# Optimization experiments

Hardware: AMD Instinct MI355X
Metric: run time of the kernel (lower is better)

## Reference

```python
import jax, jax.numpy as jnp
import numpy as np
import math

DIM_IN = 512
DIM_OUT = 512
KERNEL = 3
STYLE_DIM = 2 * 128
LIN_SCALE = 1.0 / math.sqrt(STYLE_DIM)      # EqualLinear scale (lr_mul=1)
CONV_SCALE = 1.0 / math.sqrt(DIM_IN * KERNEL ** 2)  # fan_in = dim_in * k**2 (as in source)
PAD = KERNEL // 2


def setup_inputs() -> dict:
    key = jax.random.key(0)
    ks = jax.random.split(key, 5)
    B, T = 16, 2048
    x = jax.random.normal(ks[0], (B, DIM_IN, T), dtype=jnp.float32)
    c_src = jax.random.normal(ks[1], (B, 128), dtype=jnp.float32)
    c_trg = jax.random.normal(ks[2], (B, 128), dtype=jnp.float32)
    style_w = jax.random.normal(ks[3], (DIM_IN, STYLE_DIM), dtype=jnp.float32)
    style_b = jnp.ones((DIM_IN,), dtype=jnp.float32)  # bias_init=1
    weight = jax.random.normal(ks[4], (1, DIM_OUT, DIM_IN, KERNEL), dtype=jnp.float32)
    return {"x": x, "c_src": c_src, "c_trg": c_trg,
            "style_w": style_w, "style_b": style_b, "weight": weight}


def reference(x, c_src, c_trg, style_w, style_b, weight):
    B = x.shape[0]
    # EqualLinear: style code s [B, dim_in]
    c = jnp.concatenate([c_src, c_trg], axis=-1)              # [B, 256]
    s = c @ (style_w * LIN_SCALE).T + style_b                 # [B, dim_in]
    # Modulate: w [B, dim_out, dim_in, k]
    w = CONV_SCALE * weight * s[:, None, :, None]
    # Demodulate over (dim_in, k)
    demod = jax.lax.rsqrt(jnp.sum(w * w, axis=(2, 3)) + 1e-8)  # [B, dim_out]
    w = w * demod[:, :, None, None]
    # Per-sample conv1d, padding 'same' (pad = k//2), vmapped over batch
    def conv1(xi, wi):
        # xi: [dim_in, T], wi: [dim_out, dim_in, k]
        out = jax.lax.conv_general_dilated(
            xi[None], wi, window_strides=(1,), padding=[(PAD, PAD)],
            dimension_numbers=("NCH", "OIH", "NCH"))
        return out[0]                                          # [dim_out, T]
    return jax.vmap(conv1)(x, w)                               # [B, dim_out, T]
```

## Files before the change

### kernel.cpp

```cpp
#include <hip/hip_runtime.h>
#include <cstdint>
#include <cstddef>


#define LIN_SCALE  0.0625f
#define CONV_SCALE 0.014731391f

#define B_   16
#define CIN  512
#define COUT 512
#define T_   2048
#define TP   2050

typedef __bf16 bf16x8 __attribute__((ext_vector_type(8)));
typedef float  f32x4  __attribute__((ext_vector_type(4)));
typedef unsigned short u16x8 __attribute__((ext_vector_type(8)));
typedef unsigned short u16x2 __attribute__((ext_vector_type(2)));

#define AS1 __attribute__((address_space(1)))
#define AS3 __attribute__((address_space(3)))

__device__ inline unsigned short f2bf(float f) {
  __bf16 h = (__bf16)f;
  return __builtin_bit_cast(unsigned short, h);
}

__global__ __launch_bounds__(256) void style_kernel(const float* __restrict__ c_src,
                                                    const float* __restrict__ c_trg,
                                                    const float* __restrict__ sw,
                                                    const float* __restrict__ sb,
                                                    float* __restrict__ s) {
  __shared__ float c[256];
  const int b = blockIdx.y;
  const int tid = threadIdx.x;
  c[tid] = (tid < 128) ? c_src[b * 128 + tid] : c_trg[b * 128 + tid - 128];
  __syncthreads();
  const int w = tid >> 6, lane = tid & 63;
  #pragma unroll
  for (int rr = 0; rr < 16; ++rr) {
    const int i = blockIdx.x * 64 + w * 16 + rr;
    const float* row = sw + (size_t)i * 256;
    float acc = row[lane] * c[lane] + row[lane + 64] * c[lane + 64]
              + row[lane + 128] * c[lane + 128] + row[lane + 192] * c[lane + 192];
    #pragma unroll
    for (int off = 32; off; off >>= 1) acc += __shfl_down(acc, off, 64);
    if (lane == 0) s[b * 512 + i] = acc * LIN_SCALE + sb[i];
  }
}

__global__ __launch_bounds__(256) void demod_kernel(const float* __restrict__ weight,
                                                    const float* __restrict__ s,
                                                    float* __restrict__ demod,
                                                    unsigned short* __restrict__ Wb) {
  const int o = blockIdx.x;
  const int tid = threadIdx.x;
  __shared__ float wsh[1536];
  __shared__ float svs[16 * 512];
  __shared__ float partial[16][4];

  #pragma unroll
  for (int j = tid; j < 384; j += 256)
    ((float4*)wsh)[j] = ((const float4*)(weight + (size_t)o * 1536))[j];
  #pragma unroll
  for (int j = tid; j < 2048; j += 256)
    ((float4*)svs)[j] = ((const float4*)s)[j];
  __syncthreads();

  float wr[6];
  #pragma unroll
  for (int q = 0; q < 6; ++q) wr[q] = wsh[tid * 6 + q] * CONV_SCALE;

  #pragma unroll
  for (int k = 0; k < 3; ++k) {
    u16x2 v;
    v.x = f2bf(wr[k]);
    v.y = f2bf(wr[3 + k]);
    *(u16x2*)&Wb[((size_t)(k * 512 + o)) * 512 + 2 * tid] = v;
  }

  const int lane = tid & 63, w = tid >> 6;
  float ssb[16];
  #pragma unroll
  for (int b = 0; b < 16; ++b) {
    const float s0 = svs[b * 512 + 2 * tid];
    const float s1 = svs[b * 512 + 2 * tid + 1];
    float ss = 0.f;
    #pragma unroll
    for (int q = 0; q < 3; ++q) { float v = wr[q] * s0; ss += v * v; }
    #pragma unroll
    for (int q = 3; q < 6; ++q) { float v = wr[q] * s1; ss += v * v; }
    ssb[b] = ss;
  }
  #pragma unroll
  for (int b = 0; b < 16; ++b) {
    float ss = ssb[b];
    #pragma unroll
    for (int off = 32; off; off >>= 1) ss += __shfl_down(ss, off, 64);
    if (lane == 0) partial[b][w] = ss;
  }
  __syncthreads();
  if (tid < 16)
    demod[(size_t)tid * 512 + o] =
        rsqrtf(partial[tid][0] + partial[tid][1] + partial[tid][2] + partial[tid][3] + 1e-8f);
}

__global__ __launch_bounds__(256) void transpose_kernel(const float* __restrict__ x,
                                                        const float* __restrict__ s,
                                                        unsigned short* __restrict__ xT) {
  __shared__ float tile[64][65];
  __shared__ float ss[64];
  const int b = blockIdx.z, i0 = blockIdx.y * 64, t0 = blockIdx.x * 64;
  const int tid = threadIdx.x;

  if (tid < 64) ss[tid] = s[(size_t)b * 512 + i0 + tid];

  const int lr = tid >> 4;
  const int lc = (tid & 15) * 4;
  const float* xb = x + ((size_t)b * CIN + i0) * T_ + t0;
  #pragma unroll
  for (int p = 0; p < 4; ++p) {
    const int r = p * 16 + lr;
    const float4 v = *(const float4*)(xb + (size_t)r * T_ + lc);
    tile[r][lc + 0] = v.x; tile[r][lc + 1] = v.y;
    tile[r][lc + 2] = v.z; tile[r][lc + 3] = v.w;
  }
  if (blockIdx.x == 0 && tid < 8)
    *(u16x8*)&xT[(size_t)b * TP * CIN + i0 + tid * 8] = (u16x8){0,0,0,0,0,0,0,0};
  if (blockIdx.x == gridDim.x - 1 && tid < 8)
    *(u16x8*)&xT[((size_t)b * TP + TP - 1) * CIN + i0 + tid * 8] = (u16x8){0,0,0,0,0,0,0,0};
  __syncthreads();

  const int st = tid >> 3;
  const int si = (tid & 7) * 8;
  float sv[8];
  #pragma unroll
  for (int q = 0; q < 8; ++q) sv[q] = ss[si + q];
  unsigned short* xTb = xT + ((size_t)b * TP + 1 + t0) * CIN + i0;
  #pragma unroll
  for (int p = 0; p < 2; ++p) {
    const int t = p * 32 + st;
    u16x8 v;
    #pragma unroll
    for (int q = 0; q < 8; ++q) v[q] = f2bf(tile[si + q][t] * sv[q]);
    *(u16x8*)&xTb[(size_t)t * CIN + si] = v;
  }
}

#define BM 128
#define BN 256
#define BK 32

__global__ __launch_bounds__(256, 2) void gemm_kernel(const unsigned short* __restrict__ Wb,
                                                      const unsigned short* __restrict__ xT,
                                                      const float* __restrict__ demod,
                                                      float* __restrict__ out) {
  __shared__ unsigned short lA[3 * 128 * 32];
  __shared__ unsigned short lB[258 * 32];

  const int id  = blockIdx.x;
  const int xcd = id & 7;
  const int j   = id >> 3;
  const int b   = xcd + 8 * (j >> 5);
  const int r   = j & 31;
  const int o0  = (r >> 3) * BM;
  const int t0  = (r & 7) * BN;

  const int tid  = threadIdx.x;
  const int lane = tid & 63;
  const int wm   = ((tid >> 6) & 1) * 64;
  const int wn   = (tid >> 7) * 128;
  const int rl   = lane & 15;
  const int kc   = lane >> 4;

  const unsigned short* gW = Wb + (size_t)o0 * 512;
  const unsigned short* gX = xT + ((size_t)b * TP + t0) * CIN;

  f32x4 acc[4][8];
  #pragma unroll
  for (int i = 0; i < 4; ++i)
    #pragma unroll
    for (int jj = 0; jj < 8; ++jj) acc[i][jj] = (f32x4){0.f, 0.f, 0.f, 0.f};

  for (int kk = 0; kk < 16; ++kk) {
    const int i0 = kk * 32;
    __syncthreads();
    #pragma unroll
    for (int q = 0; q < 6; ++q) {
      const int ci  = q * 256 + tid;
      const int row = ci >> 2;
      const int tap = row >> 7;
      const int ar  = row & 127;
      const int gc  = ((ci & 3) ^ ((ar >> 1) & 3)) * 8;
      __builtin_amdgcn_global_load_lds(
          (const AS1 void*)(gW + (size_t)tap * 262144 + (size_t)ar * 512 + i0 + gc),
          (AS3 void*)(&lA[ci * 8]), 16, 0, 0);
    }
    #pragma unroll
    for (int q = 0; q < 4; ++q) {
      const int ci  = q * 256 + tid;
      const int row = ci >> 2;
      const int gc  = ((ci & 3) ^ ((row >> 1) & 3)) * 8;
      __builtin_amdgcn_global_load_lds(
          (const AS1 void*)(gX + (size_t)row * CIN + i0 + gc),
          (AS3 void*)(&lB[ci * 8]), 16, 0, 0);
    }
    if (tid < 8) {
      const int ci  = 1024 + tid;
      const int row = ci >> 2;
      const int gc  = ((ci & 3) ^ ((row >> 1) & 3)) * 8;
      __builtin_amdgcn_global_load_lds(
          (const AS1 void*)(gX + (size_t)row * CIN + i0 + gc),
          (AS3 void*)(&lB[ci * 8]), 16, 0, 0);
    }
    __syncthreads();

    #pragma unroll
    for (int tap = 0; tap < 3; ++tap) {
      bf16x8 af[4], bfr[8];
      #pragma unroll
      for (int mi = 0; mi < 4; ++mi) {
        const int ra = wm + mi * 16 + rl;
        af[mi] = *(const bf16x8*)&lA[((tap * 128 + ra) * 4 + (kc ^ ((ra >> 1) & 3))) * 8];
      }
      #pragma unroll
      for (int ni = 0; ni < 8; ++ni) {
        const int rb = wn + ni * 16 + rl + tap;
        bfr[ni] = *(const bf16x8*)&lB[(rb * 4 + (kc ^ ((rb >> 1) & 3))) * 8];
      }
      #pragma unroll
      for (int mi = 0; mi < 4; ++mi)
        #pragma unroll
        for (int ni = 0; ni < 8; ++ni)
          acc[mi][ni] = __builtin_amdgcn_mfma_f32_16x16x32_bf16(af[mi], bfr[ni], acc[mi][ni], 0, 0, 0);
    }
  }

  float* ob = out + ((size_t)b * COUT + o0 + wm) * T_ + t0 + wn;
  const float* dm = demod + (size_t)b * 512 + o0 + wm;
  const int rrow = (lane >> 4) * 4;
  const int ccol = lane & 15;
  #pragma unroll
  for (int mi = 0; mi < 4; ++mi) {
    float dr[4];
    #pragma unroll
    for (int rr = 0; rr < 4; ++rr) dr[rr] = dm[mi * 16 + rrow + rr];
    #pragma unroll
    for (int ni = 0; ni < 8; ++ni)
      #pragma unroll
      for (int rr = 0; rr < 4; ++rr)
        ob[(size_t)(mi * 16 + rrow + rr) * T_ + ni * 16 + ccol] = acc[mi][ni][rr] * dr[rr];
  }
}

extern "C" void kernel_launch(void* const* d_in, const int* in_sizes, int n_in,
                              void* d_out, int out_size, void* d_ws, size_t ws_size,
                              hipStream_t stream) {
  const float* x       = (const float*)d_in[0];
  const float* c_src   = (const float*)d_in[1];
  const float* c_trg   = (const float*)d_in[2];
  const float* style_w = (const float*)d_in[3];
  const float* style_b = (const float*)d_in[4];
  const float* weight  = (const float*)d_in[5];
  float* out = (float*)d_out;

  char* ws = (char*)d_ws;
  float* s_buf          = (float*)ws;
  float* demod_buf      = (float*)(ws + 32768);
  unsigned short* Wb    = (unsigned short*)(ws + 65536);
  unsigned short* xTbuf = (unsigned short*)(ws + 65536 + 1572864);

  style_kernel<<<dim3(8, 16), 256, 0, stream>>>(c_src, c_trg, style_w, style_b, s_buf);
  demod_kernel<<<dim3(COUT), 256, 0, stream>>>(weight, s_buf, demod_buf, Wb);
  transpose_kernel<<<dim3(T_ / 64, CIN / 64, B_), 256, 0, stream>>>(x, s_buf, xTbuf);
  gemm_kernel<<<dim3(512), 256, 0, stream>>>(Wb, xTbuf, demod_buf, out);
}
```

Baseline: 181.3 us.

## Double-buffer GEMM LDS stages with 512-thread blocks and per-tap prefetch interleaving

The GEMM kernel now uses 512-thread blocks covering a 128x512 output tile and double-buffered LDS. The next k-slice's A and B tiles are fetched asynchronously, interleaved with the three tap MFMA phases, and ordered with explicit vmcnt waits and barriers. MFMA sections are raised to higher priority, and demod values are preloaded before the main loop. The aim is to hide global-to-LDS latency behind compute and reuse each weight tile over a wider time tile. In exchange, LDS use doubles, the grid halves to 256 blocks, and correctness now relies on hand-tuned waitcnt values.

```diff
diff --git a/kernel.cpp b/kernel.cpp
--- a/kernel.cpp
+++ b/kernel.cpp
@@ -147,109 +147,153 @@
 }
 
 #define BM 128
-#define BN 256
-#define BK 32
-
-__global__ __launch_bounds__(256, 2) void gemm_kernel(const unsigned short* __restrict__ Wb,
+#define BN 512
+
+#define VMCNT(n) asm volatile("s_waitcnt vmcnt(" #n ")" ::: "memory")
+#define LGKM0    asm volatile("s_waitcnt lgkmcnt(0)" ::: "memory")
+#define BAR()    __builtin_amdgcn_s_barrier()
+#define SB()     __builtin_amdgcn_sched_barrier(0)
+
+#define STAGE_B(buf, i0g)                                                     \
+  { _Pragma("unroll")                                                         \
+    for (int q = 0; q < 4; ++q) {                                             \
+      const int ci  = q * 512 + tid;                                          \
+      const int row = ci >> 2;                                                \
+      const int gc  = ((ci & 3) ^ ((row >> 1) & 3)) * 8;                      \
+      __builtin_amdgcn_global_load_lds(                                       \
+          (const AS1 void*)(gX + (size_t)row * CIN + (i0g) + gc),             \
+          (AS3 void*)(&lB[buf][ci * 8]), 16, 0, 0);                           \
+    }                                                                         \
+    if (lane == 0) {                                                          \
+      const int ci  = 2048 + wid;                                             \
+      const int row = 512 + (wid >> 2);                                       \
+      const int gc  = ((ci & 3) ^ ((row >> 1) & 3)) * 8;                      \
+      __builtin_amdgcn_global_load_lds(                                       \
+          (const AS1 void*)(gX + (size_t)row * CIN + (i0g) + gc),             \
+          (AS3 void*)(&lB[buf][ci * 8]), 16, 0, 0);                           \
+    } }
+
+#define STAGE_A(buf, i0g, q)                                                  \
+  { const int ci  = (q) * 512 + tid;                                          \
+    const int ar  = tid >> 2;                                                 \
+    const int gc  = ((ci & 3) ^ ((ar >> 1) & 3)) * 8;                         \
+    __builtin_amdgcn_global_load_lds(                                         \
+        (const AS1 void*)(gW + (size_t)(q) * 262144 + (size_t)ar * 512 + (i0g) + gc), \
+        (AS3 void*)(&lA[buf][ci * 8]), 16, 0, 0);                             \
+  }
+
+#define FRAGS(tap)                                                            \
+  bf16x8 af[4]; bf16x8 bfr[8];                                                \
+  { const unsigned short* La = &lA[cur][0];                                   \
+    const unsigned short* Lb = &lB[cur][0];                                   \
+    _Pragma("unroll")                                                         \
+    for (int mi = 0; mi < 4; ++mi) {                                          \
+      const int ra = wm + mi * 16 + rl;                                       \
+      af[mi] = *(const bf16x8*)&La[(((tap) * 128 + ra) * 4 + (kc ^ ((ra >> 1) & 3))) * 8]; \
+    }                                                                         \
+    _Pragma("unroll")                                                         \
+    for (int ni = 0; ni < 8; ++ni) {                                          \
+      const int rb = wn + ni * 16 + rl + (tap);                               \
+      bfr[ni] = *(const bf16x8*)&Lb[(rb * 4 + (kc ^ ((rb >> 1) & 3))) * 8];   \
+    } }
+
+#define MFMAS()                                                               \
+  __builtin_amdgcn_s_setprio(1);                                              \
+  _Pragma("unroll")                                                           \
+  for (int mi = 0; mi < 4; ++mi)                                              \
+    _Pragma("unroll")                                                         \
+    for (int ni = 0; ni < 8; ++ni)                                            \
+      acc[mi][ni] = __builtin_amdgcn_mfma_f32_16x16x32_bf16(af[mi], bfr[ni], acc[mi][ni], 0, 0, 0); \
+  __builtin_amdgcn_s_setprio(0);
+
+__global__ __launch_bounds__(512, 2) void gemm_kernel(const unsigned short* __restrict__ Wb,
                                                       const unsigned short* __restrict__ xT,
                                                       const float* __restrict__ demod,
                                                       float* __restrict__ out) {
-  __shared__ unsigned short lA[3 * 128 * 32];
-  __shared__ unsigned short lB[258 * 32];
+  __shared__ unsigned short lA[2][1536 * 8];
+  __shared__ unsigned short lB[2][2056 * 8];
 
   const int id  = blockIdx.x;
   const int xcd = id & 7;
   const int j   = id >> 3;
-  const int b   = xcd + 8 * (j >> 5);
-  const int r   = j & 31;
-  const int o0  = (r >> 3) * BM;
-  const int t0  = (r & 7) * BN;
+  const int b   = xcd + 8 * (j >> 4);
+  const int r   = j & 15;
+  const int o0  = (r >> 2) * BM;
+  const int t0  = (r & 3) * BN;
 
   const int tid  = threadIdx.x;
   const int lane = tid & 63;
-  const int wm   = ((tid >> 6) & 1) * 64;
-  const int wn   = (tid >> 7) * 128;
+  const int wid  = tid >> 6;
+  const int wm   = (wid & 1) * 64;
+  const int wn   = (wid >> 1) * 128;
   const int rl   = lane & 15;
   const int kc   = lane >> 4;
 
   const unsigned short* gW = Wb + (size_t)o0 * 512;
   const unsigned short* gX = xT + ((size_t)b * TP + t0) * CIN;
 
+  float dmv[16];
+  {
+    const float* dmp = demod + (size_t)b * 512 + o0 + wm + (lane >> 4) * 4;
+    #pragma unroll
+    for (int mi = 0; mi < 4; ++mi)
+      #pragma unroll
+      for (int rr = 0; rr < 4; ++rr) dmv[mi * 4 + rr] = dmp[mi * 16 + rr];
+  }
+
   f32x4 acc[4][8];
   #pragma unroll
   for (int i = 0; i < 4; ++i)
     #pragma unroll
     for (int jj = 0; jj < 8; ++jj) acc[i][jj] = (f32x4){0.f, 0.f, 0.f, 0.f};
 
-  for (int kk = 0; kk < 16; ++kk) {
-    const int i0 = kk * 32;
-    __syncthreads();
-    #pragma unroll
-    for (int q = 0; q < 6; ++q) {
-      const int ci  = q * 256 + tid;
-      const int row = ci >> 2;
-      const int tap = row >> 7;
-      const int ar  = row & 127;
-      const int gc  = ((ci & 3) ^ ((ar >> 1) & 3)) * 8;
-      __builtin_amdgcn_global_load_lds(
-          (const AS1 void*)(gW + (size_t)tap * 262144 + (size_t)ar * 512 + i0 + gc),
-          (AS3 void*)(&lA[ci * 8]), 16, 0, 0);
+  STAGE_B(0, 0);
+  STAGE_A(0, 0, 0);
+  STAGE_A(0, 0, 1);
+  STAGE_A(0, 0, 2);
+  VMCNT(2); BAR(); SB();
+
+  for (int kk = 0; kk < 15; ++kk) {
+    const int cur = kk & 1;
+    const int nxt = cur ^ 1;
+    const int i0n = (kk + 1) * 32;
+    {
+      FRAGS(0);
+      STAGE_B(nxt, i0n);
+      VMCNT(6); BAR(); SB(); LGKM0; SB();
+      MFMAS(); BAR(); SB();
     }
-    #pragma unroll
-    for (int q = 0; q < 4; ++q) {
-      const int ci  = q * 256 + tid;
-      const int row = ci >> 2;
-      const int gc  = ((ci & 3) ^ ((row >> 1) & 3)) * 8;
-      __builtin_amdgcn_global_load_lds(
-          (const AS1 void*)(gX + (size_t)row * CIN + i0 + gc),
-          (AS3 void*)(&lB[ci * 8]), 16, 0, 0);
+    {
+      FRAGS(1);
+      STAGE_A(nxt, i0n, 0);
+      STAGE_A(nxt, i0n, 1);
+      VMCNT(7); BAR(); SB(); LGKM0; SB();
+      MFMAS(); BAR(); SB();
     }
-    if (tid < 8) {
-      const int ci  = 1024 + tid;
-      const int row = ci >> 2;
-      const int gc  = ((ci & 3) ^ ((row >> 1) & 3)) * 8;
-      __builtin_amdgcn_global_load_lds(
-          (const AS1 void*)(gX + (size_t)row * CIN + i0 + gc),
-          (AS3 void*)(&lB[ci * 8]), 16, 0, 0);
+    {
+      FRAGS(2);
+      STAGE_A(nxt, i0n, 2);
+      VMCNT(2); BAR(); SB(); LGKM0; SB();
+      MFMAS(); BAR(); SB();
     }
-    __syncthreads();
-
-    #pragma unroll
-    for (int tap = 0; tap < 3; ++tap) {
-      bf16x8 af[4], bfr[8];
-      #pragma unroll
-      for (int mi = 0; mi < 4; ++mi) {
-        const int ra = wm + mi * 16 + rl;
-        af[mi] = *(const bf16x8*)&lA[((tap * 128 + ra) * 4 + (kc ^ ((ra >> 1) & 3))) * 8];
-      }
-      #pragma unroll
-      for (int ni = 0; ni < 8; ++ni) {
-        const int rb = wn + ni * 16 + rl + tap;
-        bfr[ni] = *(const bf16x8*)&lB[(rb * 4 + (kc ^ ((rb >> 1) & 3))) * 8];
-      }
-      #pragma unroll
-      for (int mi = 0; mi < 4; ++mi)
-        #pragma unroll
-        for (int ni = 0; ni < 8; ++ni)
-          acc[mi][ni] = __builtin_amdgcn_mfma_f32_16x16x32_bf16(af[mi], bfr[ni], acc[mi][ni], 0, 0, 0);
-    }
+  }
+  {
+    const int cur = 1;
+    { FRAGS(0); VMCNT(1); BAR(); SB(); LGKM0; SB(); MFMAS(); BAR(); SB(); }
+    { FRAGS(1); VMCNT(0); BAR(); SB(); LGKM0; SB(); MFMAS(); BAR(); SB(); }
+    { FRAGS(2); LGKM0; SB(); MFMAS(); }
   }
 
   float* ob = out + ((size_t)b * COUT + o0 + wm) * T_ + t0 + wn;
-  const float* dm = demod + (size_t)b * 512 + o0 + wm;
   const int rrow = (lane >> 4) * 4;
   const int ccol = lane & 15;
   #pragma unroll
-  for (int mi = 0; mi < 4; ++mi) {
-    float dr[4];
-    #pragma unroll
-    for (int rr = 0; rr < 4; ++rr) dr[rr] = dm[mi * 16 + rrow + rr];
+  for (int mi = 0; mi < 4; ++mi)
     #pragma unroll
     for (int ni = 0; ni < 8; ++ni)
       #pragma unroll
       for (int rr = 0; rr < 4; ++rr)
-        ob[(size_t)(mi * 16 + rrow + rr) * T_ + ni * 16 + ccol] = acc[mi][ni][rr] * dr[rr];
-  }
+        ob[(size_t)(mi * 16 + rrow + rr) * T_ + ni * 16 + ccol] = acc[mi][ni][rr] * dmv[mi * 4 + rr];
 }
 
 extern "C" void kernel_launch(void* const* d_in, const int* in_sizes, int n_in,
@@ -272,5 +316,5 @@
   style_kernel<<<dim3(8, 16), 256, 0, stream>>>(c_src, c_trg, style_w, style_b, s_buf);
   demod_kernel<<<dim3(COUT), 256, 0, stream>>>(weight, s_buf, demod_buf, Wb);
   transpose_kernel<<<dim3(T_ / 64, CIN / 64, B_), 256, 0, stream>>>(x, s_buf, xTbuf);
-  gemm_kernel<<<dim3(512), 256, 0, stream>>>(Wb, xTbuf, demod_buf, out);
-}
+  gemm_kernel<<<dim3(256), 512, 0, stream>>>(Wb, xTbuf, demod_buf, out);
+}
```

Result: slower. 185.0 us (+2.1%).

## Fuse style, transpose, demod and GEMM into one persistent kernel with grid barriers

Applied to the files above, without the earlier changes.

Replaces the four kernel launches with a single 512-block kernel that runs the style linear, the scaled transpose of x, the demod/weight conversion and the conv GEMM in phases. The phases are separated by software grid barriers built on atomics, plus a tiny init kernel that resets the barrier counters. This removes launch gaps and the idle tail between dependent kernels. In exchange every block must be co-resident for the barrier to complete (512 blocks at 2 per CU), the barriers spin, and the transpose work is redistributed as 8 tiles per block.

```diff
diff --git a/kernel.cpp b/kernel.cpp
--- a/kernel.cpp
+++ b/kernel.cpp
@@ -25,230 +25,253 @@
   return __builtin_bit_cast(unsigned short, h);
 }
 
-__global__ __launch_bounds__(256) void style_kernel(const float* __restrict__ c_src,
-                                                    const float* __restrict__ c_trg,
-                                                    const float* __restrict__ sw,
-                                                    const float* __restrict__ sb,
-                                                    float* __restrict__ s) {
-  __shared__ float c[256];
-  const int b = blockIdx.y;
+__global__ void init_kernel(unsigned* sync) { sync[0] = 0u; sync[1] = 0u; }
+
+__device__ inline void grid_barrier(unsigned* cnt, unsigned* gen, unsigned nb) {
+  __syncthreads();
+  if (threadIdx.x == 0) {
+    __threadfence();
+    const unsigned g = __hip_atomic_load(gen, __ATOMIC_RELAXED, __HIP_MEMORY_SCOPE_AGENT);
+    const unsigned a = __hip_atomic_fetch_add(cnt, 1u, __ATOMIC_ACQ_REL, __HIP_MEMORY_SCOPE_AGENT);
+    if (a == nb - 1u) {
+      __hip_atomic_store(cnt, 0u, __ATOMIC_RELAXED, __HIP_MEMORY_SCOPE_AGENT);
+      __hip_atomic_store(gen, g + 1u, __ATOMIC_RELEASE, __HIP_MEMORY_SCOPE_AGENT);
+    } else {
+      int t = 0;
+      while (__hip_atomic_load(gen, __ATOMIC_ACQUIRE, __HIP_MEMORY_SCOPE_AGENT) == g) {
+        __builtin_amdgcn_s_sleep(2);
+        if (++t > (1 << 24)) break;
+      }
+    }
+    __threadfence();
+  }
+  __syncthreads();
+}
+
+__global__ __launch_bounds__(256, 2) void mega_kernel(
+    const float* __restrict__ x, const float* __restrict__ c_src,
+    const float* __restrict__ c_trg, const float* __restrict__ sw,
+    const float* __restrict__ sb, const float* __restrict__ weight,
+    float* __restrict__ s, float* __restrict__ demod,
+    unsigned short* __restrict__ Wb, unsigned short* __restrict__ xT,
+    float* __restrict__ out, unsigned* __restrict__ sync) {
+  __shared__ __align__(16) char smem[41472];
+  const int id  = blockIdx.x;
   const int tid = threadIdx.x;
-  c[tid] = (tid < 128) ? c_src[b * 128 + tid] : c_trg[b * 128 + tid - 128];
+
+  if (id < 128) {
+    float* c = (float*)smem;
+    const int b = id >> 3, bx = id & 7;
+    c[tid] = (tid < 128) ? c_src[b * 128 + tid] : c_trg[b * 128 + tid - 128];
+    __syncthreads();
+    const int w = tid >> 6, lane = tid & 63;
+    #pragma unroll
+    for (int rr = 0; rr < 16; ++rr) {
+      const int i = bx * 64 + w * 16 + rr;
+      const float* row = sw + (size_t)i * 256;
+      float acc = row[lane] * c[lane] + row[lane + 64] * c[lane + 64]
+                + row[lane + 128] * c[lane + 128] + row[lane + 192] * c[lane + 192];
+      #pragma unroll
+      for (int off = 32; off; off >>= 1) acc += __shfl_down(acc, off, 64);
+      if (lane == 0) s[b * 512 + i] = acc * LIN_SCALE + sb[i];
+    }
+  }
+  grid_barrier(sync, sync + 1, gridDim.x);
+
+  {
+    float* tile = (float*)smem;
+    float* ss   = (float*)(smem + 64 * 65 * 4);
+    const int b   = id >> 5;
+    const int i0  = ((id >> 2) & 7) * 64;
+    const int t0b = (id & 3) * 512;
+    if (tid < 64) ss[tid] = s[(size_t)b * 512 + i0 + tid];
+
+    const int lr = tid >> 4;
+    const int lc = (tid & 15) * 4;
+    const int st = tid >> 3;
+    const int si = (tid & 7) * 8;
+
+    for (int u = 0; u < 8; ++u) {
+      const int t0 = t0b + u * 64;
+      if (u) __syncthreads();
+      const float* xb = x + ((size_t)b * CIN + i0) * T_ + t0;
+      #pragma unroll
+      for (int p = 0; p < 4; ++p) {
+        const int r = p * 16 + lr;
+        const float4 v = *(const float4*)(xb + (size_t)r * T_ + lc);
+        tile[r * 65 + lc + 0] = v.x; tile[r * 65 + lc + 1] = v.y;
+        tile[r * 65 + lc + 2] = v.z; tile[r * 65 + lc + 3] = v.w;
+      }
+      if (t0 == 0 && tid < 8)
+        *(u16x8*)&xT[(size_t)b * TP * CIN + i0 + tid * 8] = (u16x8){0,0,0,0,0,0,0,0};
+      if (t0 == T_ - 64 && tid < 8)
+        *(u16x8*)&xT[((size_t)b * TP + TP - 1) * CIN + i0 + tid * 8] = (u16x8){0,0,0,0,0,0,0,0};
+      __syncthreads();
+      float sv[8];
+      #pragma unroll
+      for (int q = 0; q < 8; ++q) sv[q] = ss[si + q];
+      unsigned short* xTb = xT + ((size_t)b * TP + 1 + t0) * CIN + i0;
+      #pragma unroll
+      for (int p = 0; p < 2; ++p) {
+        const int t = p * 32 + st;
+        u16x8 v;
+        #pragma unroll
+        for (int q = 0; q < 8; ++q) v[q] = f2bf(tile[(si + q) * 65 + t] * sv[q]);
+        *(u16x8*)&xTb[(size_t)t * CIN + si] = v;
+      }
+    }
+  }
   __syncthreads();
-  const int w = tid >> 6, lane = tid & 63;
-  #pragma unroll
-  for (int rr = 0; rr < 16; ++rr) {
-    const int i = blockIdx.x * 64 + w * 16 + rr;
-    const float* row = sw + (size_t)i * 256;
-    float acc = row[lane] * c[lane] + row[lane + 64] * c[lane + 64]
-              + row[lane + 128] * c[lane + 128] + row[lane + 192] * c[lane + 192];
-    #pragma unroll
-    for (int off = 32; off; off >>= 1) acc += __shfl_down(acc, off, 64);
-    if (lane == 0) s[b * 512 + i] = acc * LIN_SCALE + sb[i];
-  }
-}
-
-__global__ __launch_bounds__(256) void demod_kernel(const float* __restrict__ weight,
-                                                    const float* __restrict__ s,
-                                                    float* __restrict__ demod,
-                                                    unsigned short* __restrict__ Wb) {
-  const int o = blockIdx.x;
-  const int tid = threadIdx.x;
-  __shared__ float wsh[1536];
-  __shared__ float svs[16 * 512];
-  __shared__ float partial[16][4];
-
-  #pragma unroll
-  for (int j = tid; j < 384; j += 256)
-    ((float4*)wsh)[j] = ((const float4*)(weight + (size_t)o * 1536))[j];
-  #pragma unroll
-  for (int j = tid; j < 2048; j += 256)
-    ((float4*)svs)[j] = ((const float4*)s)[j];
-  __syncthreads();
-
-  float wr[6];
-  #pragma unroll
-  for (int q = 0; q < 6; ++q) wr[q] = wsh[tid * 6 + q] * CONV_SCALE;
-
-  #pragma unroll
-  for (int k = 0; k < 3; ++k) {
-    u16x2 v;
-    v.x = f2bf(wr[k]);
-    v.y = f2bf(wr[3 + k]);
-    *(u16x2*)&Wb[((size_t)(k * 512 + o)) * 512 + 2 * tid] = v;
-  }
-
-  const int lane = tid & 63, w = tid >> 6;
-  float ssb[16];
-  #pragma unroll
-  for (int b = 0; b < 16; ++b) {
-    const float s0 = svs[b * 512 + 2 * tid];
-    const float s1 = svs[b * 512 + 2 * tid + 1];
-    float ss = 0.f;
-    #pragma unroll
-    for (int q = 0; q < 3; ++q) { float v = wr[q] * s0; ss += v * v; }
-    #pragma unroll
-    for (int q = 3; q < 6; ++q) { float v = wr[q] * s1; ss += v * v; }
-    ssb[b] = ss;
-  }
-  #pragma unroll
-  for (int b = 0; b < 16; ++b) {
-    float ss = ssb[b];
-    #pragma unroll
-    for (int off = 32; off; off >>= 1) ss += __shfl_down(ss, off, 64);
-    if (lane == 0) partial[b][w] = ss;
-  }
-  __syncthreads();
-  if (tid < 16)
-    demod[(size_t)tid * 512 + o] =
-        rsqrtf(partial[tid][0] + partial[tid][1] + partial[tid][2] + partial[tid][3] + 1e-8f);
-}
-
-__global__ __launch_bounds__(256) void transpose_kernel(const float* __restrict__ x,
-                                                        const float* __restrict__ s,
-                                                        unsigned short* __restrict__ xT) {
-  __shared__ float tile[64][65];
-  __shared__ float ss[64];
-  const int b = blockIdx.z, i0 = blockIdx.y * 64, t0 = blockIdx.x * 64;
-  const int tid = threadIdx.x;
-
-  if (tid < 64) ss[tid] = s[(size_t)b * 512 + i0 + tid];
-
-  const int lr = tid >> 4;
-  const int lc = (tid & 15) * 4;
-  const float* xb = x + ((size_t)b * CIN + i0) * T_ + t0;
-  #pragma unroll
-  for (int p = 0; p < 4; ++p) {
-    const int r = p * 16 + lr;
-    const float4 v = *(const float4*)(xb + (size_t)r * T_ + lc);
-    tile[r][lc + 0] = v.x; tile[r][lc + 1] = v.y;
-    tile[r][lc + 2] = v.z; tile[r][lc + 3] = v.w;
-  }
-  if (blockIdx.x == 0 && tid < 8)
-    *(u16x8*)&xT[(size_t)b * TP * CIN + i0 + tid * 8] = (u16x8){0,0,0,0,0,0,0,0};
-  if (blockIdx.x == gridDim.x - 1 && tid < 8)
-    *(u16x8*)&xT[((size_t)b * TP + TP - 1) * CIN + i0 + tid * 8] = (u16x8){0,0,0,0,0,0,0,0};
-  __syncthreads();
-
-  const int st = tid >> 3;
-  const int si = (tid & 7) * 8;
-  float sv[8];
-  #pragma unroll
-  for (int q = 0; q < 8; ++q) sv[q] = ss[si + q];
-  unsigned short* xTb = xT + ((size_t)b * TP + 1 + t0) * CIN + i0;
-  #pragma unroll
-  for (int p = 0; p < 2; ++p) {
-    const int t = p * 32 + st;
-    u16x8 v;
-    #pragma unroll
-    for (int q = 0; q < 8; ++q) v[q] = f2bf(tile[si + q][t] * sv[q]);
-    *(u16x8*)&xTb[(size_t)t * CIN + si] = v;
-  }
-}
-
-#define BM 128
-#define BN 256
-#define BK 32
-
-__global__ __launch_bounds__(256, 2) void gemm_kernel(const unsigned short* __restrict__ Wb,
-                                                      const unsigned short* __restrict__ xT,
-                                                      const float* __restrict__ demod,
-                                                      float* __restrict__ out) {
-  __shared__ unsigned short lA[3 * 128 * 32];
-  __shared__ unsigned short lB[258 * 32];
-
-  const int id  = blockIdx.x;
-  const int xcd = id & 7;
-  const int j   = id >> 3;
-  const int b   = xcd + 8 * (j >> 5);
-  const int r   = j & 31;
-  const int o0  = (r >> 3) * BM;
-  const int t0  = (r & 7) * BN;
-
-  const int tid  = threadIdx.x;
-  const int lane = tid & 63;
-  const int wm   = ((tid >> 6) & 1) * 64;
-  const int wn   = (tid >> 7) * 128;
-  const int rl   = lane & 15;
-  const int kc   = lane >> 4;
-
-  const unsigned short* gW = Wb + (size_t)o0 * 512;
-  const unsigned short* gX = xT + ((size_t)b * TP + t0) * CIN;
-
-  f32x4 acc[4][8];
-  #pragma unroll
-  for (int i = 0; i < 4; ++i)
-    #pragma unroll
-    for (int jj = 0; jj < 8; ++jj) acc[i][jj] = (f32x4){0.f, 0.f, 0.f, 0.f};
-
-  for (int kk = 0; kk < 16; ++kk) {
-    const int i0 = kk * 32;
+
+  {
+    float* wsh     = (float*)smem;
+    float* svs     = (float*)(smem + 6144);
+    float* partial = (float*)(smem + 38912);
+    const int o = id;
+
+    #pragma unroll
+    for (int j = tid; j < 384; j += 256)
+      ((float4*)wsh)[j] = ((const float4*)(weight + (size_t)o * 1536))[j];
+    #pragma unroll
+    for (int j = tid; j < 2048; j += 256)
+      ((float4*)svs)[j] = ((const float4*)s)[j];
     __syncthreads();
-    #pragma unroll
-    for (int q = 0; q < 6; ++q) {
-      const int ci  = q * 256 + tid;
-      const int row = ci >> 2;
-      const int tap = row >> 7;
-      const int ar  = row & 127;
-      const int gc  = ((ci & 3) ^ ((ar >> 1) & 3)) * 8;
-      __builtin_amdgcn_global_load_lds(
-          (const AS1 void*)(gW + (size_t)tap * 262144 + (size_t)ar * 512 + i0 + gc),
-          (AS3 void*)(&lA[ci * 8]), 16, 0, 0);
-    }
-    #pragma unroll
-    for (int q = 0; q < 4; ++q) {
-      const int ci  = q * 256 + tid;
-      const int row = ci >> 2;
-      const int gc  = ((ci & 3) ^ ((row >> 1) & 3)) * 8;
-      __builtin_amdgcn_global_load_lds(
-          (const AS1 void*)(gX + (size_t)row * CIN + i0 + gc),
-          (AS3 void*)(&lB[ci * 8]), 16, 0, 0);
-    }
-    if (tid < 8) {
-      const int ci  = 1024 + tid;
-      const int row = ci >> 2;
-      const int gc  = ((ci & 3) ^ ((row >> 1) & 3)) * 8;
-      __builtin_amdgcn_global_load_lds(
-          (const AS1 void*)(gX + (size_t)row * CIN + i0 + gc),
-          (AS3 void*)(&lB[ci * 8]), 16, 0, 0);
+
+    float wr[6];
+    #pragma unroll
+    for (int q = 0; q < 6; ++q) wr[q] = wsh[tid * 6 + q] * CONV_SCALE;
+
+    #pragma unroll
+    for (int k = 0; k < 3; ++k) {
+      u16x2 v;
+      v.x = f2bf(wr[k]);
+      v.y = f2bf(wr[3 + k]);
+      *(u16x2*)&Wb[((size_t)(k * 512 + o)) * 512 + 2 * tid] = v;
+    }
+
+    const int lane = tid & 63, w = tid >> 6;
+    float ssb[16];
+    #pragma unroll
+    for (int b = 0; b < 16; ++b) {
+      const float s0 = svs[b * 512 + 2 * tid];
+      const float s1 = svs[b * 512 + 2 * tid + 1];
+      float ssq = 0.f;
+      #pragma unroll
+      for (int q = 0; q < 3; ++q) { float v = wr[q] * s0; ssq += v * v; }
+      #pragma unroll
+      for (int q = 3; q < 6; ++q) { float v = wr[q] * s1; ssq += v * v; }
+      ssb[b] = ssq;
+    }
+    #pragma unroll
+    for (int b = 0; b < 16; ++b) {
+      float ssq = ssb[b];
+      #pragma unroll
+      for (int off = 32; off; off >>= 1) ssq += __shfl_down(ssq, off, 64);
+      if (lane == 0) partial[b * 4 + w] = ssq;
     }
     __syncthreads();
-
-    #pragma unroll
-    for (int tap = 0; tap < 3; ++tap) {
-      bf16x8 af[4], bfr[8];
-      #pragma unroll
-      for (int mi = 0; mi < 4; ++mi) {
-        const int ra = wm + mi * 16 + rl;
-        af[mi] = *(const bf16x8*)&lA[((tap * 128 + ra) * 4 + (kc ^ ((ra >> 1) & 3))) * 8];
-      }
-      #pragma unroll
-      for (int ni = 0; ni < 8; ++ni) {
-        const int rb = wn + ni * 16 + rl + tap;
-        bfr[ni] = *(const bf16x8*)&lB[(rb * 4 + (kc ^ ((rb >> 1) & 3))) * 8];
-      }
-      #pragma unroll
-      for (int mi = 0; mi < 4; ++mi)
-        #pragma unroll
-        for (int ni = 0; ni < 8; ++ni)
-          acc[mi][ni] = __builtin_amdgcn_mfma_f32_16x16x32_bf16(af[mi], bfr[ni], acc[mi][ni], 0, 0, 0);
-    }
-  }
-
-  float* ob = out + ((size_t)b * COUT + o0 + wm) * T_ + t0 + wn;
-  const float* dm = demod + (size_t)b * 512 + o0 + wm;
-  const int rrow = (lane >> 4) * 4;
-  const int ccol = lane & 15;
-  #pragma unroll
-  for (int mi = 0; mi < 4; ++mi) {
-    float dr[4];
-    #pragma unroll
-    for (int rr = 0; rr < 4; ++rr) dr[rr] = dm[mi * 16 + rrow + rr];
-    #pragma unroll
-    for (int ni = 0; ni < 8; ++ni)
-      #pragma unroll
-      for (int rr = 0; rr < 4; ++rr)
-        ob[(size_t)(mi * 16 + rrow + rr) * T_ + ni * 16 + ccol] = acc[mi][ni][rr] * dr[rr];
+    if (tid < 16)
+      demod[(size_t)tid * 512 + o] =
+          rsqrtf(partial[tid * 4] + partial[tid * 4 + 1] + partial[tid * 4 + 2]
+               + partial[tid * 4 + 3] + 1e-8f);
+  }
+  grid_barrier(sync, sync + 1, gridDim.x);
+
+  {
+    unsigned short* lA = (unsigned short*)smem;
+    unsigned short* lB = (unsigned short*)(smem + 24576);
+
+    const int xcd = id & 7;
+    const int j   = id >> 3;
+    const int b   = xcd + 8 * (j >> 5);
+    const int r   = j & 31;
+    const int o0  = (r >> 3) * 128;
+    const int t0  = (r & 7) * 256;
+
+    const int lane = tid & 63;
+    const int wm   = ((tid >> 6) & 1) * 64;
+    const int wn   = (tid >> 7) * 128;
+    const int rl   = lane & 15;
+    const int kc   = lane >> 4;
+
+    const unsigned short* gW = Wb + (size_t)o0 * 512;
+    const unsigned short* gX = xT + ((size_t)b * TP + t0) * CIN;
+
+    f32x4 acc[4][8];
+    #pragma unroll
+    for (int i = 0; i < 4; ++i)
+      #pragma unroll
+      for (int jj = 0; jj < 8; ++jj) acc[i][jj] = (f32x4){0.f, 0.f, 0.f, 0.f};
+
+    for (int kk = 0; kk < 16; ++kk) {
+      const int i0 = kk * 32;
+      __syncthreads();
+      #pragma unroll
+      for (int q = 0; q < 6; ++q) {
+        const int ci  = q * 256 + tid;
+        const int row = ci >> 2;
+        const int tap = row >> 7;
+        const int ar  = row & 127;
+        const int gc  = ((ci & 3) ^ ((ar >> 1) & 3)) * 8;
+        __builtin_amdgcn_global_load_lds(
+            (const AS1 void*)(gW + (size_t)tap * 262144 + (size_t)ar * 512 + i0 + gc),
+            (AS3 void*)(&lA[ci * 8]), 16, 0, 0);
+      }
+      #pragma unroll
+      for (int q = 0; q < 4; ++q) {
+        const int ci  = q * 256 + tid;
+        const int row = ci >> 2;
+        const int gc  = ((ci & 3) ^ ((row >> 1) & 3)) * 8;
+        __builtin_amdgcn_global_load_lds(
+            (const AS1 void*)(gX + (size_t)row * CIN + i0 + gc),
+            (AS3 void*)(&lB[ci * 8]), 16, 0, 0);
+      }
+      if (tid < 8) {
+        const int ci  = 1024 + tid;
+        const int row = ci >> 2;
+        const int gc  = ((ci & 3) ^ ((row >> 1) & 3)) * 8;
+        __builtin_amdgcn_global_load_lds(
+            (const AS1 void*)(gX + (size_t)row * CIN + i0 + gc),
+            (AS3 void*)(&lB[ci * 8]), 16, 0, 0);
+      }
+      __syncthreads();
+
+      #pragma unroll
+      for (int tap = 0; tap < 3; ++tap) {
+        bf16x8 af[4], bfr[8];
+        #pragma unroll
+        for (int mi = 0; mi < 4; ++mi) {
+          const int ra = wm + mi * 16 + rl;
+          af[mi] = *(const bf16x8*)&lA[((tap * 128 + ra) * 4 + (kc ^ ((ra >> 1) & 3))) * 8];
+        }
+        #pragma unroll
+        for (int ni = 0; ni < 8; ++ni) {
+          const int rb = wn + ni * 16 + rl + tap;
+          bfr[ni] = *(const bf16x8*)&lB[(rb * 4 + (kc ^ ((rb >> 1) & 3))) * 8];
+        }
+        #pragma unroll
+        for (int mi = 0; mi < 4; ++mi)
+          #pragma unroll
+          for (int ni = 0; ni < 8; ++ni)
+            acc[mi][ni] = __builtin_amdgcn_mfma_f32_16x16x32_bf16(af[mi], bfr[ni], acc[mi][ni], 0, 0, 0);
+      }
+    }
+
+    float* ob = out + ((size_t)b * COUT + o0 + wm) * T_ + t0 + wn;
+    const float* dm = demod + (size_t)b * 512 + o0 + wm;
+    const int rrow = (lane >> 4) * 4;
+    const int ccol = lane & 15;
+    #pragma unroll
+    for (int mi = 0; mi < 4; ++mi) {
+      float dr[4];
+      #pragma unroll
+      for (int rr = 0; rr < 4; ++rr) dr[rr] = dm[mi * 16 + rrow + rr];
+      #pragma unroll
+      for (int ni = 0; ni < 8; ++ni)
+        #pragma unroll
+        for (int rr = 0; rr < 4; ++rr)
+          ob[(size_t)(mi * 16 + rrow + rr) * T_ + ni * 16 + ccol] = acc[mi][ni][rr] * dr[rr];
+    }
   }
 }
 
@@ -268,9 +291,10 @@
   float* demod_buf      = (float*)(ws + 32768);
   unsigned short* Wb    = (unsigned short*)(ws + 65536);
   unsigned short* xTbuf = (unsigned short*)(ws + 65536 + 1572864);
-
-  style_kernel<<<dim3(8, 16), 256, 0, stream>>>(c_src, c_trg, style_w, style_b, s_buf);
-  demod_kernel<<<dim3(COUT), 256, 0, stream>>>(weight, s_buf, demod_buf, Wb);
-  transpose_kernel<<<dim3(T_ / 64, CIN / 64, B_), 256, 0, stream>>>(x, s_buf, xTbuf);
-  gemm_kernel<<<dim3(512), 256, 0, stream>>>(Wb, xTbuf, demod_buf, out);
+  unsigned* sync        = (unsigned*)(ws + 35225600);
+
+  init_kernel<<<dim3(1), 1, 0, stream>>>(sync);
+  mega_kernel<<<dim3(512), 256, 0, stream>>>(x, c_src, c_trg, style_w, style_b,
+                                             weight, s_buf, demod_buf, Wb, xTbuf,
+                                             out, sync);
 }
```

Measured after the change: 356.0 us. 1.96x slower.

## Double-buffer x tile in LDS and load weights directly into registers

Applied to the files above, without the earlier changes.

The weight tile no longer goes through LDS: each wave loads its weight fragments straight from global memory into registers. The x tile is double-buffered in LDS so the next k-step's load overlaps the current MFMAs, with one barrier per iteration instead of two. Operands are swapped so the output is written as 16-byte vectors along T. The cost is more global load traffic for weights, with per-iteration latency exposed if it misses L2, and more register pressure.

```diff
diff --git a/kernel.cpp b/kernel.cpp
--- a/kernel.cpp
+++ b/kernel.cpp
@@ -146,110 +146,108 @@
   }
 }
 
-#define BM 128
-#define BN 256
-#define BK 32
+#define VMCNT0  asm volatile("s_waitcnt vmcnt(0)" ::: "memory")
+
+#define STAGEB(buf, i0g) do {                                                 \
+    _Pragma("unroll")                                                         \
+    for (int q = 0; q < 4; ++q) {                                             \
+      const int ci  = q * 256 + tid;                                          \
+      const int row = ci >> 2;                                                \
+      const int gc  = ((ci & 3) ^ ((row >> 1) & 3)) * 8;                      \
+      __builtin_amdgcn_global_load_lds(                                       \
+          (const AS1 void*)(gX + (size_t)row * CIN + (i0g) + gc),             \
+          (AS3 void*)(&lB[buf][ci * 8]), 16, 0, 0);                           \
+    }                                                                         \
+    if (tid < 8) {                                                            \
+      const int ci  = 1024 + tid;                                             \
+      const int row = ci >> 2;                                                \
+      const int gc  = ((ci & 3) ^ ((row >> 1) & 3)) * 8;                      \
+      __builtin_amdgcn_global_load_lds(                                       \
+          (const AS1 void*)(gX + (size_t)row * CIN + (i0g) + gc),             \
+          (AS3 void*)(&lB[buf][ci * 8]), 16, 0, 0);                           \
+    }                                                                         \
+  } while (0)
 
 __global__ __launch_bounds__(256, 2) void gemm_kernel(const unsigned short* __restrict__ Wb,
                                                       const unsigned short* __restrict__ xT,
                                                       const float* __restrict__ demod,
                                                       float* __restrict__ out) {
-  __shared__ unsigned short lA[3 * 128 * 32];
-  __shared__ unsigned short lB[258 * 32];
+  __shared__ unsigned short lB[2][1032 * 8];
 
   const int id  = blockIdx.x;
   const int xcd = id & 7;
   const int j   = id >> 3;
   const int b   = xcd + 8 * (j >> 5);
   const int r   = j & 31;
-  const int o0  = (r >> 3) * BM;
-  const int t0  = (r & 7) * BN;
+  const int o0  = (r >> 3) * 128;
+  const int t0  = (r & 7) * 256;
 
   const int tid  = threadIdx.x;
   const int lane = tid & 63;
-  const int wm   = ((tid >> 6) & 1) * 64;
-  const int wn   = (tid >> 7) * 128;
+  const int wt   = ((tid >> 6) & 1) * 128;
+  const int wo   = (tid >> 7) * 64;
   const int rl   = lane & 15;
   const int kc   = lane >> 4;
 
-  const unsigned short* gW = Wb + (size_t)o0 * 512;
-  const unsigned short* gX = xT + ((size_t)b * TP + t0) * CIN;
-
-  f32x4 acc[4][8];
-  #pragma unroll
-  for (int i = 0; i < 4; ++i)
-    #pragma unroll
-    for (int jj = 0; jj < 8; ++jj) acc[i][jj] = (f32x4){0.f, 0.f, 0.f, 0.f};
+  const unsigned short* gWl = Wb + ((size_t)(o0 + wo + rl)) * 512 + kc * 8;
+  const unsigned short* gX  = xT + ((size_t)b * TP + t0) * CIN;
+
+  f32x4 acc[8][4];
+  #pragma unroll
+  for (int i = 0; i < 8; ++i)
+    #pragma unroll
+    for (int jj = 0; jj < 4; ++jj) acc[i][jj] = (f32x4){0.f, 0.f, 0.f, 0.f};
+
+  STAGEB(0, 0);
+  VMCNT0;
+  __builtin_amdgcn_s_barrier();
 
   for (int kk = 0; kk < 16; ++kk) {
-    const int i0 = kk * 32;
-    __syncthreads();
-    #pragma unroll
-    for (int q = 0; q < 6; ++q) {
-      const int ci  = q * 256 + tid;
-      const int row = ci >> 2;
-      const int tap = row >> 7;
-      const int ar  = row & 127;
-      const int gc  = ((ci & 3) ^ ((ar >> 1) & 3)) * 8;
-      __builtin_amdgcn_global_load_lds(
-          (const AS1 void*)(gW + (size_t)tap * 262144 + (size_t)ar * 512 + i0 + gc),
-          (AS3 void*)(&lA[ci * 8]), 16, 0, 0);
-    }
-    #pragma unroll
-    for (int q = 0; q < 4; ++q) {
-      const int ci  = q * 256 + tid;
-      const int row = ci >> 2;
-      const int gc  = ((ci & 3) ^ ((row >> 1) & 3)) * 8;
-      __builtin_amdgcn_global_load_lds(
-          (const AS1 void*)(gX + (size_t)row * CIN + i0 + gc),
-          (AS3 void*)(&lB[ci * 8]), 16, 0, 0);
-    }
-    if (tid < 8) {
-      const int ci  = 1024 + tid;
-      const int row = ci >> 2;
-      const int gc  = ((ci & 3) ^ ((row >> 1) & 3)) * 8;
-      __builtin_amdgcn_global_load_lds(
-          (const AS1 void*)(gX + (size_t)row * CIN + i0 + gc),
-          (AS3 void*)(&lB[ci * 8]), 16, 0, 0);
-    }
-    __syncthreads();
+    const int i0  = kk * 32;
+    const int cur = kk & 1;
+    if (kk < 15) STAGEB(cur ^ 1, i0 + 32);
+
+    bf16x8 wf[3][4];
+    #pragma unroll
+    for (int tap = 0; tap < 3; ++tap)
+      #pragma unroll
+      for (int ni = 0; ni < 4; ++ni)
+        wf[tap][ni] = *(const bf16x8*)(gWl + (size_t)tap * 262144 + ni * 8192 + i0);
 
     #pragma unroll
     for (int tap = 0; tap < 3; ++tap) {
-      bf16x8 af[4], bfr[8];
+      bf16x8 xf[8];
       #pragma unroll
-      for (int mi = 0; mi < 4; ++mi) {
-        const int ra = wm + mi * 16 + rl;
-        af[mi] = *(const bf16x8*)&lA[((tap * 128 + ra) * 4 + (kc ^ ((ra >> 1) & 3))) * 8];
+      for (int mi = 0; mi < 8; ++mi) {
+        const int rb = wt + mi * 16 + rl + tap;
+        xf[mi] = *(const bf16x8*)&lB[cur][(rb * 4 + (kc ^ ((rb >> 1) & 3))) * 8];
       }
       #pragma unroll
-      for (int ni = 0; ni < 8; ++ni) {
-        const int rb = wn + ni * 16 + rl + tap;
-        bfr[ni] = *(const bf16x8*)&lB[(rb * 4 + (kc ^ ((rb >> 1) & 3))) * 8];
-      }
-      #pragma unroll
-      for (int mi = 0; mi < 4; ++mi)
+      for (int mi = 0; mi < 8; ++mi)
         #pragma unroll
-        for (int ni = 0; ni < 8; ++ni)
-          acc[mi][ni] = __builtin_amdgcn_mfma_f32_16x16x32_bf16(af[mi], bfr[ni], acc[mi][ni], 0, 0, 0);
+        for (int ni = 0; ni < 4; ++ni)
+          acc[mi][ni] = __builtin_amdgcn_mfma_f32_16x16x32_bf16(xf[mi], wf[tap][ni], acc[mi][ni], 0, 0, 0);
     }
-  }
-
-  float* ob = out + ((size_t)b * COUT + o0 + wm) * T_ + t0 + wn;
-  const float* dm = demod + (size_t)b * 512 + o0 + wm;
-  const int rrow = (lane >> 4) * 4;
+
+    VMCNT0;
+    __builtin_amdgcn_s_barrier();
+  }
+
   const int ccol = lane & 15;
-  #pragma unroll
-  for (int mi = 0; mi < 4; ++mi) {
-    float dr[4];
-    #pragma unroll
-    for (int rr = 0; rr < 4; ++rr) dr[rr] = dm[mi * 16 + rrow + rr];
-    #pragma unroll
-    for (int ni = 0; ni < 8; ++ni)
-      #pragma unroll
-      for (int rr = 0; rr < 4; ++rr)
-        ob[(size_t)(mi * 16 + rrow + rr) * T_ + ni * 16 + ccol] = acc[mi][ni][rr] * dr[rr];
-  }
+  const int trow = (lane >> 4) * 4;
+  float dmv[4];
+  #pragma unroll
+  for (int ni = 0; ni < 4; ++ni)
+    dmv[ni] = demod[(size_t)b * 512 + o0 + wo + ni * 16 + ccol];
+  float* ob = out + ((size_t)b * COUT + o0 + wo + ccol) * T_ + t0 + wt + trow;
+  #pragma unroll
+  for (int mi = 0; mi < 8; ++mi)
+    #pragma unroll
+    for (int ni = 0; ni < 4; ++ni) {
+      f32x4 v = acc[mi][ni];
+      v.x *= dmv[ni]; v.y *= dmv[ni]; v.z *= dmv[ni]; v.w *= dmv[ni];
+      *(f32x4*)&ob[(size_t)ni * 16 * T_ + mi * 16] = v;
+    }
 }
 
 extern "C" void kernel_launch(void* const* d_in, const int* in_sizes, int n_in,
```

New measurement: 196.6 us. +8.5%, slower.
